# Performance work log

Measured on AMD Instinct MI355X. Metric: run time of the kernel, lower is better.

Reference implementation:

```python
import jax, jax.numpy as jnp
import numpy as np

V, N, C, H, Wd = 12, 80000, 256, 128, 128  # views, points, feat dim, feat map HxW
G, M, E, L = 4096, 512, 200000, 20         # groups, masks, mask-point pairs, labels


def setup_inputs() -> dict:
    key = jax.random.key(0)
    ks = jax.random.split(key, 10)
    img_feat = jax.random.normal(ks[0], (V, C, H, Wd), dtype=jnp.float32)
    coords = jax.random.randint(ks[1], (V, N, 2), 0, H)              # pixel (x, y) per point per view
    is_seen = jax.random.uniform(ks[2], (V, N), dtype=jnp.float32)   # view visibility weights
    centers = jax.random.randint(ks[3], (G,), 0, N)                  # group center point indices
    group2mask = jax.random.randint(ks[4], (G,), 0, M)               # group -> mask assignment
    pair_mask = jax.random.randint(ks[5], (E,), 0, M)                # flattened mask_pc_ind: mask ids
    pair_point = jax.random.randint(ks[6], (E,), 0, N)               # flattened mask_pc_ind: point ids
    W1 = jax.random.normal(ks[7], (C, C // 2), dtype=jnp.float32) / np.sqrt(C).astype(np.float32)
    b1 = jnp.zeros((C // 2,), jnp.float32)
    W2 = jax.random.normal(ks[8], (C // 2, L), dtype=jnp.float32) / np.sqrt(C // 2).astype(np.float32)
    b2 = jnp.zeros((L,), jnp.float32)
    return dict(img_feat=img_feat, is_seen=is_seen, W1=W1, b1=b1, W2=W2, b2=b2,
                coords=coords, centers=centers, group2mask=group2mask,
                pair_mask=pair_mask, pair_point=pair_point)


def reference(img_feat, is_seen, W1, b1, W2, b2, coords, centers, group2mask, pair_mask, pair_point):
    # --- aggregate(): multi-view pixel gather + visibility-weighted mean over views ---
    x = coords[..., 0]  # [V, N]
    y = coords[..., 1]  # [V, N]
    vidx = jnp.arange(V)[:, None]
    point_feats = img_feat[vidx, :, y, x]  # [V, N, C] (advanced indexing puts C last)
    pc_feat = jnp.sum(point_feats * is_seen[:, :, None], axis=0) / (
        jnp.sum(is_seen, axis=0)[:, None] + 1e-6)  # [N, C]

    # --- compute_avg_features_from_grouped(): segment-mean of group feats into masks ---
    group_feat = pc_feat[centers]  # [G, C]
    msum = jax.ops.segment_sum(group_feat, group2mask, num_segments=M)          # [M, C]
    mcnt = jax.ops.segment_sum(jnp.ones((G,), pc_feat.dtype), group2mask, num_segments=M)
    mask_feat = jnp.where(mcnt[:, None] > 0, msum / jnp.maximum(mcnt, 1.0)[:, None], 0.0)

    # --- simple_down(): scatter_add mask feats back to points, count-normalized ---
    all_feats = mask_feat[pair_mask]  # [E, C]
    fsum = jax.ops.segment_sum(all_feats, pair_point, num_segments=N)           # [N, C]
    cnt = jax.ops.segment_sum(jnp.ones((E,), pc_feat.dtype), pair_point, num_segments=N)
    pc_feat_ave = fsum / jnp.maximum(cnt, 1e-6)[:, None]  # [N, C]

    # --- classifier: Linear(C, C/2) -> ReLU -> (Dropout eval=identity) -> Linear(C/2, L) ---
    h = jax.nn.relu(pc_feat_ave @ W1 + b1)
    logits = h @ W2 + b2  # [N, L]
    return logits
```

## Files before the change

kernel.cpp:

```cpp
#include <hip/hip_runtime.h>

#define V_ 12
#define N_ 80000
#define C_ 256
#define H_ 128
#define W_ 128
#define G_ 4096
#define M_ 512
#define E_ 200000
#define L_ 20
#define HD 128
#define NROW (V_ * H_)
#define RCAP 128
#define PCAP 32
#define MCAP 64
#define GV (G_ * V_)
#define GSEG (G_ * 16)
#define QCH 64
#define NZERO (M_ + NROW + N_)

__global__ void init_kernel(float4* __restrict__ z) {
  int i = blockIdx.x * blockDim.x + threadIdx.x;
  if (i < NZERO / 4) z[i] = make_float4(0.f, 0.f, 0.f, 0.f);
}

__global__ void build_kernel(const float* __restrict__ is_seen,
                             const int* __restrict__ coords,
                             const int* __restrict__ centers,
                             const int* __restrict__ g2m,
                             const int* __restrict__ pair_mask,
                             const int* __restrict__ pair_point,
                             int* __restrict__ rcount,
                             int* __restrict__ rmeta,
                             float* __restrict__ rscale,
                             int* __restrict__ pcount,
                             int* __restrict__ pitems,
                             int* __restrict__ mgcnt,
                             int* __restrict__ mitems) {
  int t = blockIdx.x * blockDim.x + threadIdx.x;
  if (t < GSEG) {
    int g = t >> 4;
    int s = t & 15;
    int n = centers[g];
    float w = 0.f;
    int x = 0, y = 0;
    if (s < V_) {
      w = is_seen[(size_t)s * N_ + n];
      int2 xy = ((const int2*)coords)[(size_t)s * N_ + n];
      x = xy.x; y = xy.y;
    }
    float wsum = w;
    wsum += __shfl_xor(wsum, 1, 16);
    wsum += __shfl_xor(wsum, 2, 16);
    wsum += __shfl_xor(wsum, 4, 16);
    wsum += __shfl_xor(wsum, 8, 16);
    int m = g2m[g];
    if (s == 0) {
      int slot = atomicAdd(&mgcnt[m], 1);
      if (slot < MCAP) mitems[m * MCAP + slot] = g;
    }
    if (s < V_) {
      float sc = w / (wsum + 1e-6f);
      int b = (s << 7) | y;
      int slot = atomicAdd(&rcount[b], 1);
      if (slot < RCAP) {
        rmeta[b * RCAP + slot] = g | (x << 12);
        rscale[b * RCAP + slot] = sc;
      }
    }
  } else if (t < GSEG + E_) {
    int e = t - GSEG;
    int p = pair_point[e];
    int slot = atomicAdd(&pcount[p], 1);
    if (slot < PCAP) pitems[(size_t)p * PCAP + slot] = pair_mask[e];
  }
}

__global__ void gather_kernel(const float* __restrict__ img,
                              const int* __restrict__ rcount,
                              const int* __restrict__ rmeta,
                              const float* __restrict__ rscale,
                              float* __restrict__ pvg) {
  int bid = blockIdx.x;
  int b = bid >> 2;
  int cg = bid & 3;
  int cnt = rcount[b];
  if (cnt == 0) return;
  if (cnt > RCAP) cnt = RCAP;
  int v = b >> 7;
  int y = b & 127;
  int t = threadIdx.x;
  __shared__ float rows[QCH * 129];
  const float4* base = (const float4*)(img +
      (((size_t)v * C_ + cg * QCH) * H_ + y) * W_);
#pragma unroll
  for (int i = 0; i < 8; ++i) {
    int f4 = i * 256 + t;
    int ch = f4 >> 5;
    int xo4 = f4 & 31;
    float4 u = base[(size_t)ch * (H_ * W_ / 4) + xo4];
    float* dst = &rows[ch * 129 + xo4 * 4];
    dst[0] = u.x; dst[1] = u.y; dst[2] = u.z; dst[3] = u.w;
  }
  __syncthreads();
  int w = t >> 6;
  int lane = t & 63;
  for (int it = w; it < cnt; it += 4) {
    int meta = rmeta[b * RCAP + it];
    float s = rscale[b * RCAP + it];
    int g = meta & 4095;
    int x = (meta >> 12) & 127;
    float val = rows[lane * 129 + x] * s;
    pvg[((size_t)g * V_ + v) * C_ + cg * QCH + lane] = val;
  }
}

__global__ void maskw1_kernel(const float* __restrict__ pvg,
                              const int* __restrict__ mgcnt,
                              const int* __restrict__ mitems,
                              const float* __restrict__ W1,
                              float* __restrict__ mW1) {
  int m = blockIdx.x;
  int t = threadIdx.x;
  __shared__ float row[C_];
  __shared__ float pbuf[256];
  int cnt = mgcnt[m];
  int k = cnt < MCAP ? cnt : MCAP;
  float acc = 0.f;
  for (int kg = 0; kg < k; ++kg) {
    int g = mitems[m * MCAP + kg];
    const float* base = pvg + (size_t)g * V_ * C_ + t;
#pragma unroll
    for (int v = 0; v < V_; ++v) acc += base[v * C_];
  }
  row[t] = acc;
  __syncthreads();
  int j = t & 127;
  int half = t >> 7;
  float part = 0.f;
  const float* w1b = W1 + (size_t)half * 128 * HD + j;
  const float* rowb = row + half * 128;
#pragma unroll 4
  for (int c = 0; c < 128; ++c) part += rowb[c] * w1b[(size_t)c * HD];
  pbuf[t] = part;
  __syncthreads();
  if (t < HD) {
    float inv = 1.0f / fmaxf((float)cnt, 1.0f);
    mW1[(size_t)m * HD + t] = (pbuf[t] + pbuf[t + 128]) * inv;
  }
}

__global__ void point_mlp_kernel(const int* __restrict__ pcount,
                                 const int* __restrict__ pitems,
                                 const float* __restrict__ mW1,
                                 const float* __restrict__ b1,
                                 const float* __restrict__ W2,
                                 const float* __restrict__ b2,
                                 float* __restrict__ out) {
  __shared__ float w2t[L_][132];
  __shared__ float hl[4][3][132];
  int t = threadIdx.x;
  for (int i = t; i < HD * L_; i += 256) {
    int kk = i / L_;
    int j = i - kk * L_;
    w2t[j][kk] = W2[i];
  }
  __syncthreads();
  int wave = t >> 6;
  int lane = t & 63;
  int pbase = blockIdx.x * 12 + wave * 3;
  float2 b1v = ((const float2*)b1)[lane];
#pragma unroll
  for (int pt = 0; pt < 3; ++pt) {
    int p = pbase + pt;
    if (p < N_) {
      int cnt = pcount[p];
      int k = cnt < PCAP ? cnt : PCAP;
      const int* lst = &pitems[(size_t)p * PCAP];
      int4 m4 = *(const int4*)lst;
      float2 r0 = make_float2(0.f, 0.f), r1 = r0, r2 = r0, r3 = r0;
      if (k > 0) r0 = ((const float2*)(mW1 + (size_t)m4.x * HD))[lane];
      if (k > 1) r1 = ((const float2*)(mW1 + (size_t)m4.y * HD))[lane];
      if (k > 2) r2 = ((const float2*)(mW1 + (size_t)m4.z * HD))[lane];
      if (k > 3) r3 = ((const float2*)(mW1 + (size_t)m4.w * HD))[lane];
      float hx = r0.x + r1.x + r2.x + r3.x;
      float hy = r0.y + r1.y + r2.y + r3.y;
      for (int it = 4; it < k; ++it) {
        int m = lst[it];
        float2 r = ((const float2*)(mW1 + (size_t)m * HD))[lane];
        hx += r.x;
        hy += r.y;
      }
      float invc = 1.0f / fmaxf((float)cnt, 1e-6f);
      hl[wave][pt][2 * lane]     = fmaxf(hx * invc + b1v.x, 0.f);
      hl[wave][pt][2 * lane + 1] = fmaxf(hy * invc + b1v.y, 0.f);
    }
  }
  __syncthreads();
  if (lane < 60) {
    int pt = lane / 20;
    int j  = lane - pt * 20;
    int p = pbase + pt;
    if (p < N_) {
      float o = b2[j];
      const float4* h4 = (const float4*)&hl[wave][pt][0];
      const float4* w4 = (const float4*)&w2t[j][0];
#pragma unroll
      for (int q = 0; q < HD / 4; ++q) {
        float4 hv = h4[q];
        float4 wv = w4[q];
        o += hv.x * wv.x + hv.y * wv.y + hv.z * wv.z + hv.w * wv.w;
      }
      out[(size_t)p * L_ + j] = o;
    }
  }
}

extern "C" void kernel_launch(void* const* d_in, const int* in_sizes, int n_in,
                              void* d_out, int out_size, void* d_ws, size_t ws_size,
                              hipStream_t stream) {
  const float* img      = (const float*)d_in[0];
  const float* is_seen  = (const float*)d_in[1];
  const float* W1       = (const float*)d_in[2];
  const float* b1       = (const float*)d_in[3];
  const float* W2       = (const float*)d_in[4];
  const float* b2       = (const float*)d_in[5];
  const int* coords     = (const int*)d_in[6];
  const int* centers    = (const int*)d_in[7];
  const int* g2m        = (const int*)d_in[8];
  const int* pair_mask  = (const int*)d_in[9];
  const int* pair_point = (const int*)d_in[10];
  float* out = (float*)d_out;

  int*   mgcnt  = (int*)d_ws;
  int*   rcount = mgcnt + M_;
  int*   pcount = rcount + NROW;
  int*   mitems = pcount + N_;
  float* mW1    = (float*)(mitems + (size_t)M_ * MCAP);
  float* rscale = mW1 + (size_t)M_ * HD;
  int*   rmeta  = (int*)(rscale + (size_t)NROW * RCAP);
  int*   pitems = rmeta + (size_t)NROW * RCAP;
  float* pvg    = (float*)(pitems + (size_t)N_ * PCAP);

  init_kernel<<<(NZERO / 4 + 255) / 256, 256, 0, stream>>>((float4*)mgcnt);
  build_kernel<<<(GSEG + E_ + 255) / 256, 256, 0, stream>>>(
      is_seen, coords, centers, g2m, pair_mask, pair_point,
      rcount, rmeta, rscale, pcount, pitems, mgcnt, mitems);
  gather_kernel<<<NROW * 4, 256, 0, stream>>>(img, rcount, rmeta, rscale, pvg);
  maskw1_kernel<<<M_, 256, 0, stream>>>(pvg, mgcnt, mitems, W1, mW1);
  point_mlp_kernel<<<(N_ + 11) / 12, 256, 0, stream>>>(
      pcount, pitems, mW1, b1, W2, b2, out);
}
```

Baseline: 125.9 us.

## Accumulate per-group view sums atomically and widen gather and MLP blocks

The gather kernel now atomically adds view-weighted pixel features into a per-group [G,C] buffer instead of writing a [G,V,C] intermediate. This removes the 12x larger intermediate write and the per-view re-read in the mask kernel, at the cost of float atomics and zeroing 4 MB more in init. Both the gather and the point MLP kernels move to 512-thread blocks, and the MLP processes 24 points per block with a shared second-layer stage. The MLP also drops the __syncthreads between staging W2 into shared memory and its first use. That is safe only because of the later barrier before w2t is read.

New measurement: 125.3 us. About the same (-0.5%).

```diff
diff --git a/kernel.cpp b/kernel.cpp
--- a/kernel.cpp
+++ b/kernel.cpp
@@ -14,10 +14,10 @@
 #define RCAP 128
 #define PCAP 32
 #define MCAP 64
-#define GV (G_ * V_)
 #define GSEG (G_ * 16)
 #define QCH 64
-#define NZERO (M_ + NROW + N_)
+#define MLP_PTS 24
+#define NZERO (G_ * C_ + M_ + NROW + N_)
 
 __global__ void init_kernel(float4* __restrict__ z) {
   int i = blockIdx.x * blockDim.x + threadIdx.x;
@@ -76,11 +76,12 @@
   }
 }
 
-__global__ void gather_kernel(const float* __restrict__ img,
-                              const int* __restrict__ rcount,
-                              const int* __restrict__ rmeta,
-                              const float* __restrict__ rscale,
-                              float* __restrict__ pvg) {
+__global__ void __launch_bounds__(512)
+gather_kernel(const float* __restrict__ img,
+              const int* __restrict__ rcount,
+              const int* __restrict__ rmeta,
+              const float* __restrict__ rscale,
+              float* __restrict__ gsum) {
   int bid = blockIdx.x;
   int b = bid >> 2;
   int cg = bid & 3;
@@ -94,8 +95,8 @@
   const float4* base = (const float4*)(img +
       (((size_t)v * C_ + cg * QCH) * H_ + y) * W_);
 #pragma unroll
-  for (int i = 0; i < 8; ++i) {
-    int f4 = i * 256 + t;
+  for (int i = 0; i < 4; ++i) {
+    int f4 = i * 512 + t;
     int ch = f4 >> 5;
     int xo4 = f4 & 31;
     float4 u = base[(size_t)ch * (H_ * W_ / 4) + xo4];
@@ -105,17 +106,17 @@
   __syncthreads();
   int w = t >> 6;
   int lane = t & 63;
-  for (int it = w; it < cnt; it += 4) {
+  for (int it = w; it < cnt; it += 8) {
     int meta = rmeta[b * RCAP + it];
     float s = rscale[b * RCAP + it];
     int g = meta & 4095;
     int x = (meta >> 12) & 127;
     float val = rows[lane * 129 + x] * s;
-    pvg[((size_t)g * V_ + v) * C_ + cg * QCH + lane] = val;
-  }
-}
-
-__global__ void maskw1_kernel(const float* __restrict__ pvg,
+    atomicAdd(&gsum[(size_t)g * C_ + cg * QCH + lane], val);
+  }
+}
+
+__global__ void maskw1_kernel(const float* __restrict__ gsum,
                               const int* __restrict__ mgcnt,
                               const int* __restrict__ mitems,
                               const float* __restrict__ W1,
@@ -129,9 +130,7 @@
   float acc = 0.f;
   for (int kg = 0; kg < k; ++kg) {
     int g = mitems[m * MCAP + kg];
-    const float* base = pvg + (size_t)g * V_ * C_ + t;
-#pragma unroll
-    for (int v = 0; v < V_; ++v) acc += base[v * C_];
+    acc += gsum[(size_t)g * C_ + t];
   }
   row[t] = acc;
   __syncthreads();
@@ -150,29 +149,30 @@
   }
 }
 
-__global__ void point_mlp_kernel(const int* __restrict__ pcount,
-                                 const int* __restrict__ pitems,
-                                 const float* __restrict__ mW1,
-                                 const float* __restrict__ b1,
-                                 const float* __restrict__ W2,
-                                 const float* __restrict__ b2,
-                                 float* __restrict__ out) {
+__global__ void __launch_bounds__(512)
+point_mlp_kernel(const int* __restrict__ pcount,
+                 const int* __restrict__ pitems,
+                 const float* __restrict__ mW1,
+                 const float* __restrict__ b1,
+                 const float* __restrict__ W2,
+                 const float* __restrict__ b2,
+                 float* __restrict__ out) {
   __shared__ float w2t[L_][132];
-  __shared__ float hl[4][3][132];
+  __shared__ float hl[MLP_PTS][132];
   int t = threadIdx.x;
-  for (int i = t; i < HD * L_; i += 256) {
+  for (int i = t; i < HD * L_; i += 512) {
     int kk = i / L_;
     int j = i - kk * L_;
     w2t[j][kk] = W2[i];
   }
-  __syncthreads();
   int wave = t >> 6;
   int lane = t & 63;
-  int pbase = blockIdx.x * 12 + wave * 3;
+  int pbase = blockIdx.x * MLP_PTS;
   float2 b1v = ((const float2*)b1)[lane];
 #pragma unroll
   for (int pt = 0; pt < 3; ++pt) {
-    int p = pbase + pt;
+    int lp = wave * 3 + pt;
+    int p = pbase + lp;
     if (p < N_) {
       int cnt = pcount[p];
       int k = cnt < PCAP ? cnt : PCAP;
@@ -192,18 +192,18 @@
         hy += r.y;
       }
       float invc = 1.0f / fmaxf((float)cnt, 1e-6f);
-      hl[wave][pt][2 * lane]     = fmaxf(hx * invc + b1v.x, 0.f);
-      hl[wave][pt][2 * lane + 1] = fmaxf(hy * invc + b1v.y, 0.f);
-    }
-  }
-  __syncthreads();
-  if (lane < 60) {
-    int pt = lane / 20;
-    int j  = lane - pt * 20;
+      hl[lp][2 * lane]     = fmaxf(hx * invc + b1v.x, 0.f);
+      hl[lp][2 * lane + 1] = fmaxf(hy * invc + b1v.y, 0.f);
+    }
+  }
+  __syncthreads();
+  if (t < MLP_PTS * L_) {
+    int pt = t / L_;
+    int j  = t - pt * L_;
     int p = pbase + pt;
     if (p < N_) {
       float o = b2[j];
-      const float4* h4 = (const float4*)&hl[wave][pt][0];
+      const float4* h4 = (const float4*)&hl[pt][0];
       const float4* w4 = (const float4*)&w2t[j][0];
 #pragma unroll
       for (int q = 0; q < HD / 4; ++q) {
@@ -232,7 +232,8 @@
   const int* pair_point = (const int*)d_in[10];
   float* out = (float*)d_out;
 
-  int*   mgcnt  = (int*)d_ws;
+  float* gsum   = (float*)d_ws;
+  int*   mgcnt  = (int*)(gsum + (size_t)G_ * C_);
   int*   rcount = mgcnt + M_;
   int*   pcount = rcount + NROW;
   int*   mitems = pcount + N_;
@@ -240,14 +241,13 @@
   float* rscale = mW1 + (size_t)M_ * HD;
   int*   rmeta  = (int*)(rscale + (size_t)NROW * RCAP);
   int*   pitems = rmeta + (size_t)NROW * RCAP;
-  float* pvg    = (float*)(pitems + (size_t)N_ * PCAP);
-
-  init_kernel<<<(NZERO / 4 + 255) / 256, 256, 0, stream>>>((float4*)mgcnt);
+
+  init_kernel<<<(NZERO / 4 + 255) / 256, 256, 0, stream>>>((float4*)gsum);
   build_kernel<<<(GSEG + E_ + 255) / 256, 256, 0, stream>>>(
       is_seen, coords, centers, g2m, pair_mask, pair_point,
       rcount, rmeta, rscale, pcount, pitems, mgcnt, mitems);
-  gather_kernel<<<NROW * 4, 256, 0, stream>>>(img, rcount, rmeta, rscale, pvg);
-  maskw1_kernel<<<M_, 256, 0, stream>>>(pvg, mgcnt, mitems, W1, mW1);
-  point_mlp_kernel<<<(N_ + 11) / 12, 256, 0, stream>>>(
+  gather_kernel<<<NROW * 4, 512, 0, stream>>>(img, rcount, rmeta, rscale, gsum);
+  maskw1_kernel<<<M_, 256, 0, stream>>>(gsum, mgcnt, mitems, W1, mW1);
+  point_mlp_kernel<<<(N_ + MLP_PTS - 1) / MLP_PTS, 512, 0, stream>>>(
       pcount, pitems, mW1, b1, W2, b2, out);
 }
```
